# Kernel optimization log

Hardware: AMD Instinct MI355X
Metric: run time of the kernel (lower is better)

The kernel has to match this reference:

```python
import jax, jax.numpy as jnp
import numpy as np

N, D, E = 200000, 256, 6400000
RATIO = 0.5
NEG_SLOPE = 0.2


def _xavier(key, shape, gain=1.414):
    fan_in, fan_out = shape[0], shape[1]
    limit = gain * (6.0 / (fan_in + fan_out)) ** 0.5
    return jax.random.uniform(key, shape, jnp.float32, -limit, limit)


def setup_inputs() -> dict:
    key = jax.random.key(0)
    ks = jax.random.split(key, 8)
    x = jax.random.normal(ks[0], (N, D), jnp.float32)
    edge_index = jax.random.randint(ks[1], (2, E), 0, N, dtype=jnp.int64)
    return {
        "x": x,
        "edge_index": edge_index,
        "w_s1": _xavier(ks[2], (2 * D, D)), "b_s1": jnp.zeros((D,), jnp.float32),
        "w_s2": _xavier(ks[3], (D, 1)),     "b_s2": jnp.zeros((1,), jnp.float32),
        "w_f1": _xavier(ks[4], (D, D // 2)), "b_f1": jnp.zeros((D // 2,), jnp.float32),
        "w_f2": _xavier(ks[5], (D // 2, 1)), "b_f2": jnp.zeros((1,), jnp.float32),
        "w_p": _xavier(ks[6], (D, D)),      "b_p": jnp.zeros((D,), jnp.float32),
        "alpha": jnp.float32(0.5), "beta": jnp.float32(0.5),
    }


def reference(x, edge_index, w_s1, b_s1, w_s2, b_s2, w_f1, b_f1, w_f2, b_f2, w_p, b_p, alpha, beta):
    num_nodes = x.shape[0]
    k = max(1, int(RATIO * num_nodes))
    lrelu = lambda v: jax.nn.leaky_relu(v, NEG_SLOPE)

    row, col = edge_index[0], edge_index[1]
    # degree(row, N): scatter-add of ones over source nodes
    deg = jax.ops.segment_sum(jnp.ones_like(row, dtype=x.dtype), row, num_segments=num_nodes)
    # F.normalize(p=2, dim=0) on the [N,1] degree column
    deg_norm = deg / jnp.maximum(jnp.sqrt(jnp.sum(deg * deg)), 1e-12)

    struct_in = jnp.concatenate([x, jnp.broadcast_to(deg_norm[:, None], x.shape)], axis=1)  # [N, 2D]
    struct_scores = (lrelu(struct_in @ w_s1 + b_s1) @ w_s2 + b_s2)[:, 0]  # dropout is eval no-op
    feat_scores = (lrelu(x @ w_f1 + b_f1) @ w_f2 + b_f2)[:, 0]

    a = jax.nn.sigmoid(alpha)
    b = jax.nn.sigmoid(beta)
    s = a + b
    scores = (a / s) * struct_scores + (b / s) * feat_scores  # [N]

    # single-graph top-k (batch=None default path)
    topk_scores, topk_idx = jax.lax.top_k(scores, k)
    x_pooled = lrelu(x[topk_idx] @ w_p + b_p)  # post_pool, dropout no-op

    # edge remap + compaction (valid edges first, -1 padding to keep static shape)
    node_map = jnp.full((num_nodes,), -1, dtype=jnp.int32).at[topk_idx].set(
        jnp.arange(k, dtype=jnp.int32))
    mr, mc = node_map[row], node_map[col]
    mask = (mr >= 0) & (mc >= 0)
    order = jnp.argsort(~mask, stable=True)  # stable: keeps original edge order among valid
    edge_index_pooled = jnp.stack([
        jnp.where(mask, mr, -1)[order],
        jnp.where(mask, mc, -1)[order],
    ])
    return x_pooled, edge_index_pooled, topk_scores
```

## Files before the change

### kernel.cpp

```cpp
#include <hip/hip_runtime.h>
#include <math.h>

typedef unsigned long long u64;
typedef unsigned int u32;
typedef unsigned short u16;
typedef __attribute__((ext_vector_type(8))) short bf16x8;
typedef __attribute__((ext_vector_type(4))) float f32x4;

#define D   256
#define ECH 16
#define EBLK (256*ECH)
#define BAND_W 2048
#define BAND_DELTA 1e-3f
#define HR  50176
#define HCH 64
#define NBUCK 65536

__device__ __forceinline__ double lrelu(double v){ return v > 0.0 ? v : 0.2*v; }
__device__ __forceinline__ float  lreluf(float v){ return v > 0.0f ? v : 0.2f*v; }

__device__ __forceinline__ u16 f2bf(float f){
  union{float f; u32 u;} v; v.f = f;
  u32 r = v.u + 0x7FFFu + ((v.u >> 16) & 1u);
  return (u16)(r >> 16);
}
__device__ __forceinline__ float bf2f(u16 b){
  union{u32 u; float f;} v; v.u = ((u32)b) << 16; return v.f;
}

__global__ __launch_bounds__(256) void k_deghist(const int* __restrict__ row, int E,
                                                 u32* __restrict__ partial, int NR){
  __shared__ u32 h[HR/4];
  const int tid = threadIdx.x;
  const int r = blockIdx.x % NR;
  const int c = blockIdx.x / NR;
  for (int i = tid; i < HR/4; i += 256) h[i] = 0;
  __syncthreads();
  const int lo = r * HR;
  int CE = ((E + HCH - 1) / HCH + 3) & ~3;
  const int e0 = c * CE;
  const int e1 = min(e0 + CE, E);
  for (int e = e0 + tid*4; e < e1; e += 256*4){
    if (e + 3 < e1){
      int4 v = *(const int4*)(row + e);
      u32 d0 = (u32)(v.x - lo), d1 = (u32)(v.y - lo);
      u32 d2 = (u32)(v.z - lo), d3 = (u32)(v.w - lo);
      if (d0 < (u32)HR) atomicAdd(&h[d0 >> 2], 1u << ((d0 & 3)*8));
      if (d1 < (u32)HR) atomicAdd(&h[d1 >> 2], 1u << ((d1 & 3)*8));
      if (d2 < (u32)HR) atomicAdd(&h[d2 >> 2], 1u << ((d2 & 3)*8));
      if (d3 < (u32)HR) atomicAdd(&h[d3 >> 2], 1u << ((d3 & 3)*8));
    } else {
      for (int j = 0; j < 4 && e + j < e1; ++j){
        u32 d = (u32)(row[e+j] - lo);
        if (d < (u32)HR) atomicAdd(&h[d >> 2], 1u << ((d & 3)*8));
      }
    }
  }
  __syncthreads();
  u32* plane = partial + (size_t)blockIdx.x * (HR/4);
  for (int i = tid; i < HR/4; i += 256) plane[i] = h[i];
}

__global__ void k_degred2(const u32* __restrict__ partial, int N, int NR,
                          int* __restrict__ deg, u64* __restrict__ out){
  __shared__ u64 sh[256];
  u64 local = 0;
  int stride = gridDim.x*blockDim.x;
  for (int i = blockIdx.x*blockDim.x + threadIdx.x; i < N; i += stride){
    int r = i / HR, off = i % HR;
    const int word = off >> 2, shift = (off & 3)*8;
    u32 s = 0;
    #pragma unroll 8
    for (int c = 0; c < HCH; ++c)
      s += (partial[(size_t)(c*NR + r)*(HR/4) + word] >> shift) & 0xFFu;
    deg[i] = (int)s;
    local += (u64)s * (u64)s;
  }
  sh[threadIdx.x] = local; __syncthreads();
  for (int s = 128; s > 0; s >>= 1){
    if (threadIdx.x < s) sh[threadIdx.x] += sh[threadIdx.x+s];
    __syncthreads();
  }
  if (threadIdx.x == 0) atomicAdd(out, sh[0]);
}

__global__ void k_prep_wsw(const float* __restrict__ wS1, const float* __restrict__ wF1,
                           const float* __restrict__ wP,
                           const float* __restrict__ alpha, const float* __restrict__ beta,
                           const u64* __restrict__ sumsq,
                           u16* __restrict__ wswH, u16* __restrict__ wswL,
                           u16* __restrict__ wPH,
                           double* __restrict__ s1b, double* __restrict__ scal,
                           float* __restrict__ s1bf, float* __restrict__ scalf){
  const int b = blockIdx.x;
  if (b < 384){
    int idx = b*256 + threadIdx.x;
    int i    = idx & 7;
    int lane = (idx >> 3) & 63;
    int sg   = (idx >> 9) & 7;
    int t    = idx >> 12;
    int k = sg*32 + ((lane >> 4) & 3)*8 + i;
    int c16 = lane & 15;
    float wv;
    if (t < 16) wv = wS1[k*256 + t*16 + c16];
    else        wv = wF1[k*128 + (t-16)*16 + c16];
    u16 h = f2bf(wv);
    wswH[idx] = h;
    wswL[idx] = f2bf(wv - bf2f(h));
  } else if (b < 640){
    int idx = (b-384)*256 + threadIdx.x;
    int i    = idx & 7;
    int lane = (idx >> 3) & 63;
    int sg   = (idx >> 9) & 7;
    int t    = idx >> 12;
    int k = sg*32 + ((lane >> 4) & 3)*8 + i;
    wPH[idx] = f2bf(wP[k*256 + t*16 + (lane & 15)]);
  } else {
    int j = threadIdx.x;
    double s = 0.0;
    for (int r = 0; r < D; ++r) s += (double)wS1[(D + r)*D + j];
    s1b[j] = s;
    s1bf[j] = (float)s;
    if (j == 0){
      double a = 1.0/(1.0 + exp(-(double)alpha[0]));
      double bb = 1.0/(1.0 + exp(-(double)beta[0]));
      scal[0] = a/(a+bb);
      scal[1] = bb/(a+bb);
      double dn = sqrt((double)(*sumsq));
      scal[2] = dn > 1e-12 ? dn : 1e-12;
      scalf[0] = (float)scal[0];
      scalf[1] = (float)scal[1];
      scalf[2] = (float)(1.0/scal[2]);
    }
  }
}

__global__ __launch_bounds__(512, 4) void k_scores_mfma(
    const float* __restrict__ x, const int* __restrict__ deg,
    const u16* __restrict__ wswH, const u16* __restrict__ wswL,
    const float* __restrict__ bS1, const float* __restrict__ wS2, const float* __restrict__ bS2,
    const float* __restrict__ bF1, const float* __restrict__ wF2, const float* __restrict__ bF2,
    const float* __restrict__ s1bf, const float* __restrict__ scalf,
    float* __restrict__ s32, u64* __restrict__ keysrc, u32* __restrict__ kmm, int N)
{
  __shared__ u16 xsh[2][4096];
  __shared__ u16 xsl[2][4096];
  __shared__ float dnsh[64];
  __shared__ float part_s[64][9];
  __shared__ float part_f[64][9];

  const int tid  = threadIdx.x;
  const int lane = tid & 63;
  const int w    = tid >> 6;
  const int node0 = blockIdx.x * 64;

  if (tid < 64){
    int node = node0 + tid;
    dnsh[tid] = (node < N) ? ((float)deg[node] * scalf[2]) : 0.0f;
  }

  const int row_st = tid >> 3;
  const int seg_st = tid & 7;
  const int unit_w = row_st*8 + (seg_st ^ (row_st & 7));
  const float* srcbase = x + (size_t)(node0 + row_st)*D + seg_st*8;
  const bool rv = (node0 + row_st) < N;

  f32x4 acc[4][3];
  #pragma unroll
  for (int m = 0; m < 4; ++m)
    #pragma unroll
    for (int n = 0; n < 3; ++n) acc[m][n] = (f32x4){0.f,0.f,0.f,0.f};

  float xr[8];
  {
    if (rv){
      float4 a = *(const float4*)(srcbase);
      float4 b = *(const float4*)(srcbase + 4);
      xr[0]=a.x; xr[1]=a.y; xr[2]=a.z; xr[3]=a.w;
      xr[4]=b.x; xr[5]=b.y; xr[6]=b.z; xr[7]=b.w;
    } else {
      #pragma unroll
      for (int i = 0; i < 8; ++i) xr[i] = 0.f;
    }
  }

  #pragma unroll
  for (int c = 0; c < 4; ++c){
    const int pb = c & 1;
    {
      u16 h[8];
      #pragma unroll
      for (int i = 0; i < 8; ++i) h[i] = f2bf(xr[i]);
      uint4 H; H.x = (u32)h[0] | ((u32)h[1]<<16); H.y = (u32)h[2] | ((u32)h[3]<<16);
               H.z = (u32)h[4] | ((u32)h[5]<<16); H.w = (u32)h[6] | ((u32)h[7]<<16);
      u16 l[8];
      #pragma unroll
      for (int i = 0; i < 8; ++i) l[i] = f2bf(xr[i] - bf2f(h[i]));
      uint4 L; L.x = (u32)l[0] | ((u32)l[1]<<16); L.y = (u32)l[2] | ((u32)l[3]<<16);
               L.z = (u32)l[4] | ((u32)l[5]<<16); L.w = (u32)l[6] | ((u32)l[7]<<16);
      *(uint4*)&xsh[pb][unit_w*8] = H;
      *(uint4*)&xsl[pb][unit_w*8] = L;
    }
    __syncthreads();
    if (c < 3){
      const float* sn = srcbase + (c+1)*64;
      if (rv){
        float4 a = *(const float4*)(sn);
        float4 b = *(const float4*)(sn + 4);
        xr[0]=a.x; xr[1]=a.y; xr[2]=a.z; xr[3]=a.w;
        xr[4]=b.x; xr[5]=b.y; xr[6]=b.z; xr[7]=b.w;
      }
    }
    #pragma unroll
    for (int s = 0; s < 2; ++s){
      const int sg = c*2 + s;
      bf16x8 ah[4], al[4];
      #pragma unroll
      for (int mt = 0; mt < 4; ++mt){
        int row = mt*16 + (lane & 15);
        int seg = s*4 + (lane >> 4);
        int un  = row*8 + (seg ^ (row & 7));
        ah[mt] = *(const bf16x8*)&xsh[pb][un*8];
        al[mt] = *(const bf16x8*)&xsl[pb][un*8];
      }
      const int t0 = w*3;
      size_t o0 = ((size_t)(t0*8 + sg)*64 + lane)*8;
      bf16x8 bh = *(const bf16x8*)&wswH[o0];
      bf16x8 bl = *(const bf16x8*)&wswL[o0];
      #pragma unroll
      for (int nt = 0; nt < 3; ++nt){
        bf16x8 nbh = bh, nbl = bl;
        if (nt < 2){
          size_t on = ((size_t)((t0+nt+1)*8 + sg)*64 + lane)*8;
          nbh = *(const bf16x8*)&wswH[on];
          nbl = *(const bf16x8*)&wswL[on];
        }
        #pragma unroll
        for (int mt = 0; mt < 4; ++mt){
          acc[mt][nt] = __builtin_amdgcn_mfma_f32_16x16x32_bf16(ah[mt], bh, acc[mt][nt], 0,0,0);
          acc[mt][nt] = __builtin_amdgcn_mfma_f32_16x16x32_bf16(al[mt], bh, acc[mt][nt], 0,0,0);
          acc[mt][nt] = __builtin_amdgcn_mfma_f32_16x16x32_bf16(ah[mt], bl, acc[mt][nt], 0,0,0);
        }
        bh = nbh; bl = nbl;
      }
    }
    if (c < 3) __syncthreads();
  }

  float dnl[4][4];
  #pragma unroll
  for (int mt = 0; mt < 4; ++mt)
    #pragma unroll
    for (int j = 0; j < 4; ++j)
      dnl[mt][j] = dnsh[mt*16 + (lane>>4)*4 + j];

  float ps[4][4], pf[4][4];
  #pragma unroll
  for (int mt = 0; mt < 4; ++mt)
    #pragma unroll
    for (int j = 0; j < 4; ++j){ ps[mt][j] = 0.f; pf[mt][j] = 0.f; }

  #pragma unroll
  for (int nt = 0; nt < 3; ++nt){
    const int t = w*3 + nt;
    const int c16 = lane & 15;
    const bool isS = (t < 16);
    const int col = isS ? t*16 + c16 : (t-16)*16 + c16;
    const float bias = isS ? bS1[col] : bF1[col];
    const float sbv  = isS ? s1bf[col] : 0.f;
    const float vv   = isS ? wS2[col] : wF2[col];
    #pragma unroll
    for (int mt = 0; mt < 4; ++mt){
      #pragma unroll
      for (int j = 0; j < 4; ++j){
        float v = acc[mt][nt][j] + bias + dnl[mt][j]*sbv;
        v = lreluf(v) * vv;
        v += __shfl_xor(v, 1);
        v += __shfl_xor(v, 2);
        v += __shfl_xor(v, 4);
        v += __shfl_xor(v, 8);
        if (isS) ps[mt][j] += v; else pf[mt][j] += v;
      }
    }
  }
  if ((lane & 15) == 0){
    #pragma unroll
    for (int mt = 0; mt < 4; ++mt)
      #pragma unroll
      for (int j = 0; j < 4; ++j){
        int row = mt*16 + (lane>>4)*4 + j;
        part_s[row][w] = ps[mt][j];
        part_f[row][w] = pf[mt][j];
      }
  }
  __syncthreads();
  if (tid < 64){
    int node = node0 + tid;
    u32 key32mn = 0xFFFFFFFFu, key32mx = 0u;
    if (node < N){
      float sv = 0.f, fv = 0.f;
      #pragma unroll
      for (int ww = 0; ww < 8; ++ww){ sv += part_s[tid][ww]; fv += part_f[tid][ww]; }
      float sc = scalf[0]*(sv + bS2[0]) + scalf[1]*(fv + bF2[0]);
      s32[node] = sc;
      u32 bits = __float_as_uint(sc);
      u32 ord = (bits >> 31) ? ~bits : (bits | 0x80000000u);
      u32 key32 = ~ord;
      keysrc[node] = ((u64)key32 << 32) | (u32)node;
      key32mn = key32; key32mx = key32;
    }
    #pragma unroll
    for (int off = 32; off > 0; off >>= 1){
      u32 on = __shfl_xor(key32mn, off);
      u32 ox = __shfl_xor(key32mx, off);
      key32mn = min(key32mn, on);
      key32mx = max(key32mx, ox);
    }
    if (tid == 0){
      atomicMin(&kmm[0], key32mn);
      atomicMax(&kmm[1], key32mx);
    }
  }
}

__global__ void k_hist(const u64* __restrict__ keysrc, int N,
                       const u32* __restrict__ kmm, u32* __restrict__ hist){
  const u32 kmin = kmm[0];
  const u64 rng = (u64)(kmm[1] - kmm[0]) + 1;
  int stride = gridDim.x*blockDim.x;
  for (int i = blockIdx.x*blockDim.x + threadIdx.x; i < N; i += stride){
    u32 key = (u32)(keysrc[i] >> 32);
    u32 b = (u32)((((u64)(key - kmin)) << 16) / rng);
    atomicAdd(&hist[b], 1u);
  }
}

__global__ __launch_bounds__(1024) void k_scan64k(const u32* __restrict__ hist,
                                                  u32* __restrict__ boff){
  __shared__ u32 ts[1024];
  const int t = threadIdx.x;
  u32 loc[64];
  u32 s = 0;
  const uint4* hp = (const uint4*)(hist + t*64);
  #pragma unroll
  for (int i = 0; i < 16; ++i){
    uint4 v = hp[i];
    loc[i*4+0]=v.x; loc[i*4+1]=v.y; loc[i*4+2]=v.z; loc[i*4+3]=v.w;
    s += v.x + v.y + v.z + v.w;
  }
  ts[t] = s; __syncthreads();
  for (int d = 1; d < 1024; d <<= 1){
    u32 v = (t >= d) ? ts[t-d] : 0;
    __syncthreads();
    ts[t] += v;
    __syncthreads();
  }
  u32 run = ts[t] - s;
  u32* bp = boff + t*64;
  #pragma unroll 8
  for (int i = 0; i < 64; ++i){ bp[i] = run; run += loc[i]; }
}

__global__ void k_scatter(const u64* __restrict__ keysrc, int N,
                          const u32* __restrict__ kmm, u32* __restrict__ boff,
                          u64* __restrict__ keyS){
  const u32 kmin = kmm[0];
  const u64 rng = (u64)(kmm[1] - kmm[0]) + 1;
  int stride = gridDim.x*blockDim.x;
  for (int i = blockIdx.x*blockDim.x + threadIdx.x; i < N; i += stride){
    u64 kv = keysrc[i];
    u32 key = (u32)(kv >> 32);
    u32 b = (u32)((((u64)(key - kmin)) << 16) / rng);
    u32 pos = atomicAdd(&boff[b], 1u);
    keyS[pos] = kv;
  }
}

__global__ void kr_cut(const u64* __restrict__ keys, int k, float* __restrict__ cutbuf,
                       int* __restrict__ r01){
  if (threadIdx.x == 0 && blockIdx.x == 0){
    u32 key32 = (u32)(keys[k-1] >> 32);
    u32 ord = ~key32;
    u32 u = (ord & 0x80000000u) ? (ord ^ 0x80000000u) : ~ord;
    float c = __uint_as_float(u);
    cutbuf[0] = c - BAND_DELTA;
    cutbuf[1] = c + BAND_DELTA;
    r01[0] = 0x7FFFFFFF;
    r01[1] = -1;
  }
}

__global__ __launch_bounds__(256) void kr_rescore(
    const u64* __restrict__ keys, const float* __restrict__ s32,
    const float* __restrict__ x, const int* __restrict__ deg,
    const float* __restrict__ wS1, const float* __restrict__ bS1,
    const float* __restrict__ wS2, const float* __restrict__ bS2,
    const float* __restrict__ wF1, const float* __restrict__ bF1,
    const float* __restrict__ wF2, const float* __restrict__ bF2,
    const double* __restrict__ s1b, const double* __restrict__ scal,
    const float* __restrict__ cutbuf, int* __restrict__ r01,
    double* __restrict__ bandS, int k, int N)
{
  const int r = k - BAND_W + blockIdx.x;
  if (r < 0 || r >= N) return;
  const int node = (int)(u32)(keys[r] & 0xFFFFFFFFULL);
  const float s = s32[node];
  if (s < cutbuf[0] || s > cutbuf[1]){
    if (threadIdx.x == 0) bandS[blockIdx.x] = (double)s;
    return;
  }

  const int tid = threadIdx.x;
  if (tid == 0){ atomicMin(&r01[0], r); atomicMax(&r01[1], r); }

  __shared__ float xr[256];
  __shared__ double rsp[4], rfp[4];
  xr[tid] = x[(size_t)node*D + tid];
  __syncthreads();

  const int j = tid;
  double a0=0.0, a1=0.0, a2=0.0, a3=0.0;
  double b0=0.0, b1=0.0, b2=0.0, b3=0.0;
  if (j < 128){
    for (int rr = 0; rr < D; rr += 4){
      double x0 = (double)xr[rr+0], x1 = (double)xr[rr+1];
      double x2 = (double)xr[rr+2], x3 = (double)xr[rr+3];
      a0 = fma(x0, (double)wS1[(rr+0)*D + j], a0);
      a1 = fma(x1, (double)wS1[(rr+1)*D + j], a1);
      a2 = fma(x2, (double)wS1[(rr+2)*D + j], a2);
      a3 = fma(x3, (double)wS1[(rr+3)*D + j], a3);
      b0 = fma(x0, (double)wF1[(rr+0)*128 + j], b0);
      b1 = fma(x1, (double)wF1[(rr+1)*128 + j], b1);
      b2 = fma(x2, (double)wF1[(rr+2)*128 + j], b2);
      b3 = fma(x3, (double)wF1[(rr+3)*128 + j], b3);
    }
  } else {
    for (int rr = 0; rr < D; rr += 4){
      double x0 = (double)xr[rr+0], x1 = (double)xr[rr+1];
      double x2 = (double)xr[rr+2], x3 = (double)xr[rr+3];
      a0 = fma(x0, (double)wS1[(rr+0)*D + j], a0);
      a1 = fma(x1, (double)wS1[(rr+1)*D + j], a1);
      a2 = fma(x2, (double)wS1[(rr+2)*D + j], a2);
      a3 = fma(x3, (double)wS1[(rr+3)*D + j], a3);
    }
  }
  double accA = ((a0+a1)+(a2+a3)) + (double)bS1[j] + ((double)deg[node]/scal[2]) * s1b[j];
  double sp = lrelu(accA) * (double)wS2[j];
  double fp = 0.0;
  if (j < 128){
    double accB = ((b0+b1)+(b2+b3)) + (double)bF1[j];
    fp = lrelu(accB) * (double)wF2[j];
  }

  const int lane = tid & 63, wave = tid >> 6;
  #pragma unroll
  for (int off = 32; off > 0; off >>= 1){
    sp += __shfl_down(sp, off);
    fp += __shfl_down(fp, off);
  }
  if (lane == 0){ rsp[wave] = sp; rfp[wave] = fp; }
  __syncthreads();
  if (tid == 0){
    double SP = rsp[0]+rsp[1]+rsp[2]+rsp[3];
    double FP = rfp[0]+rfp[1]+rfp[2]+rfp[3];
    bandS[blockIdx.x] = scal[0]*(SP + (double)bS2[0]) + scal[1]*(FP + (double)bF2[0]);
  }
}

__global__ __launch_bounds__(1024) void kr_bandsort(u64* __restrict__ keys,
    const double* __restrict__ bandS, const int* __restrict__ r01, int k){
  __shared__ double bs[4096];
  __shared__ int bi[4096];
  const int r0 = r01[0], r1 = r01[1];
  int nb = r1 - r0 + 1;
  if (nb <= 1) return;
  if (nb > 4096) nb = 4096;
  int M = 1; while (M < nb) M <<= 1;
  const int tid = threadIdx.x;
  const int sbase = r0 - (k - BAND_W);
  for (int m = tid; m < M; m += 1024){
    if (m < nb){ bs[m] = bandS[sbase + m]; bi[m] = (int)(u32)(keys[r0+m] & 0xFFFFFFFFULL); }
    else       { bs[m] = -1.0/0.0;         bi[m] = 0x7FFFFFFF; }
  }
  __syncthreads();
  for (int size = 2; size <= M; size <<= 1){
    for (int stride = size >> 1; stride > 0; stride >>= 1){
      for (int p = tid; p < (M >> 1); p += 1024){
        int i = 2*p - (p & (stride-1));
        int jj = i + stride;
        bool up = ((i & size) == 0);
        double si_ = bs[i], sj = bs[jj];
        int ii = bi[i], ij = bi[jj];
        bool gt = (si_ < sj) || (si_ == sj && ii > ij);
        if (gt == up){ bs[i]=sj; bs[jj]=si_; bi[i]=ij; bi[jj]=ii; }
      }
      __syncthreads();
    }
  }
  for (int m = tid; m < nb; m += 1024)
    keys[r0+m] = (u64)(u32)bi[m];
}

__global__ void k_finalize(const u64* __restrict__ keys, const float* __restrict__ s32,
                           int k, int* __restrict__ nmap, float* __restrict__ outS){
  int p = blockIdx.x*blockDim.x + threadIdx.x;
  if (p < k){
    int node = (int)(u32)(keys[p] & 0xFFFFFFFFULL);
    nmap[node] = p;
    outS[p] = s32[node];
  }
}

__global__ __launch_bounds__(512, 4) void k_xpool_mfma(
    const float* __restrict__ x, const u64* __restrict__ keys,
    const u16* __restrict__ wH,
    const float* __restrict__ bP, float* __restrict__ out, int kk)
{
  __shared__ u16 xsh[2][4096];

  const int tid  = threadIdx.x;
  const int lane = tid & 63;
  const int w    = tid >> 6;
  const int p0 = blockIdx.x * 64;
  if (p0 >= kk) return;

  const int row_st = tid >> 3;
  const int seg_st = tid & 7;
  const int unit_w = row_st*8 + (seg_st ^ (row_st & 7));
  int prow = p0 + row_st; if (prow >= kk) prow = kk - 1;
  const int node = (int)(u32)(keys[prow] & 0xFFFFFFFFULL);
  const float* srcbase = x + (size_t)node*D + seg_st*8;

  f32x4 acc[4][2];
  #pragma unroll
  for (int m = 0; m < 4; ++m){ acc[m][0] = (f32x4){0.f,0.f,0.f,0.f}; acc[m][1] = (f32x4){0.f,0.f,0.f,0.f}; }

  float xr[8];
  {
    float4 a = *(const float4*)(srcbase);
    float4 b = *(const float4*)(srcbase + 4);
    xr[0]=a.x; xr[1]=a.y; xr[2]=a.z; xr[3]=a.w;
    xr[4]=b.x; xr[5]=b.y; xr[6]=b.z; xr[7]=b.w;
  }

  #pragma unroll
  for (int c = 0; c < 4; ++c){
    const int pb = c & 1;
    {
      u16 h[8];
      #pragma unroll
      for (int i = 0; i < 8; ++i) h[i] = f2bf(xr[i]);
      uint4 H; H.x = (u32)h[0] | ((u32)h[1]<<16); H.y = (u32)h[2] | ((u32)h[3]<<16);
               H.z = (u32)h[4] | ((u32)h[5]<<16); H.w = (u32)h[6] | ((u32)h[7]<<16);
      *(uint4*)&xsh[pb][unit_w*8] = H;
    }
    __syncthreads();
    if (c < 3){
      const float* sn = srcbase + (c+1)*64;
      float4 a = *(const float4*)(sn);
      float4 b = *(const float4*)(sn + 4);
      xr[0]=a.x; xr[1]=a.y; xr[2]=a.z; xr[3]=a.w;
      xr[4]=b.x; xr[5]=b.y; xr[6]=b.z; xr[7]=b.w;
    }
    #pragma unroll
    for (int s = 0; s < 2; ++s){
      const int sg = c*2 + s;
      bf16x8 ah[4];
      #pragma unroll
      for (int mt = 0; mt < 4; ++mt){
        int row = mt*16 + (lane & 15);
        int seg = s*4 + (lane >> 4);
        int un  = row*8 + (seg ^ (row & 7));
        ah[mt] = *(const bf16x8*)&xsh[pb][un*8];
      }
      const int t0 = w*2;
      size_t o0 = ((size_t)(t0*8 + sg)*64 + lane)*8;
      bf16x8 bh = *(const bf16x8*)&wH[o0];
      #pragma unroll
      for (int nt = 0; nt < 2; ++nt){
        bf16x8 nbh = bh;
        if (nt < 1){
          size_t on = ((size_t)((t0+1)*8 + sg)*64 + lane)*8;
          nbh = *(const bf16x8*)&wH[on];
        }
        #pragma unroll
        for (int mt = 0; mt < 4; ++mt)
          acc[mt][nt] = __builtin_amdgcn_mfma_f32_16x16x32_bf16(ah[mt], bh, acc[mt][nt], 0,0,0);
        bh = nbh;
      }
    }
    if (c < 3) __syncthreads();
  }

  const int c16 = lane & 15, r4 = (lane >> 4)*4;
  #pragma unroll
  for (int nt = 0; nt < 2; ++nt){
    const int col = (w*2 + nt)*16 + c16;
    const float bias = bP[col];
    #pragma unroll
    for (int mt = 0; mt < 4; ++mt){
      #pragma unroll
      for (int j = 0; j < 4; ++j){
        int p = p0 + mt*16 + r4 + j;
        if (p < kk) out[(size_t)p*D + col] = lreluf(acc[mt][nt][j] + bias);
      }
    }
  }
}

__global__ __launch_bounds__(256) void k_ecount(const int* __restrict__ erow, const int* __restrict__ ecol,
    const int* __restrict__ nmap, int E, int* __restrict__ bcount){
  __shared__ int sc[256];
  const int tid = threadIdx.x;
  const int base = blockIdx.x*EBLK + tid*ECH;
  int cnt = 0;
  #pragma unroll
  for (int q = 0; q < ECH; ++q){
    int e = base + q;
    if (e < E){
      if (nmap[erow[e]] >= 0 && nmap[ecol[e]] >= 0) cnt++;
    }
  }
  sc[tid] = cnt; __syncthreads();
  for (int s = 128; s > 0; s >>= 1){
    if (tid < s) sc[tid] += sc[tid+s];
    __syncthreads();
  }
  if (tid == 0) bcount[blockIdx.x] = sc[0];
}

__global__ __launch_bounds__(1024) void k_escan(const int* __restrict__ bcount, int nblk,
                                                int* __restrict__ boff, int* __restrict__ tot){
  __shared__ int sh[1024];
  const int tid = threadIdx.x;
  int carry = 0;
  for (int s = 0; s < nblk; s += 1024){
    int v = (s + tid < nblk) ? bcount[s+tid] : 0;
    sh[tid] = v; __syncthreads();
    for (int d = 1; d < 1024; d <<= 1){
      int t = (tid >= d) ? sh[tid-d] : 0;
      __syncthreads();
      sh[tid] += t;
      __syncthreads();
    }
    if (s + tid < nblk) boff[s+tid] = carry + sh[tid] - v;
    carry += sh[1023];
    __syncthreads();
  }
  if (tid == 0) *tot = carry;
}

__global__ void k_efill_tail(float* __restrict__ outR, float* __restrict__ outC,
                             const int* __restrict__ tot, int E){
  const int t0 = *tot;
  int stride = gridDim.x*blockDim.x;
  for (int i = t0 + blockIdx.x*blockDim.x + threadIdx.x; i < E; i += stride){
    outR[i] = -1.0f;
    outC[i] = -1.0f;
  }
}

__global__ __launch_bounds__(256) void k_escatter(const int* __restrict__ erow, const int* __restrict__ ecol,
    const int* __restrict__ nmap, int E, const int* __restrict__ boff,
    float* __restrict__ outR, float* __restrict__ outC){
  __shared__ int sc[256];
  const int tid = threadIdx.x;
  const int base = blockIdx.x*EBLK + tid*ECH;
  int mr[ECH], mc[ECH];
  int cnt = 0;
  #pragma unroll
  for (int q = 0; q < ECH; ++q){
    int e = base + q;
    int a = -1, b = -1;
    if (e < E){ a = nmap[erow[e]]; b = nmap[ecol[e]]; }
    mr[q] = a; mc[q] = b;
    if (a >= 0 && b >= 0) cnt++;
  }
  sc[tid] = cnt; __syncthreads();
  int v = cnt;
  for (int d = 1; d < 256; d <<= 1){
    int t = (tid >= d) ? sc[tid-d] : 0;
    __syncthreads();
    sc[tid] += t;
    __syncthreads();
  }
  int pos = boff[blockIdx.x] + sc[tid] - v;
  #pragma unroll
  for (int q = 0; q < ECH; ++q){
    if (mr[q] >= 0 && mc[q] >= 0){
      outR[pos] = (float)mr[q];
      outC[pos] = (float)mc[q];
      pos++;
    }
  }
}

extern "C" void kernel_launch(void* const* d_in, const int* in_sizes, int n_in,
                              void* d_out, int out_size, void* d_ws, size_t ws_size,
                              hipStream_t stream)
{
  const float* x   = (const float*)d_in[0];
  const int*   ei  = (const int*)d_in[1];
  const float* wS1 = (const float*)d_in[2];
  const float* bS1 = (const float*)d_in[3];
  const float* wS2 = (const float*)d_in[4];
  const float* bS2 = (const float*)d_in[5];
  const float* wF1 = (const float*)d_in[6];
  const float* bF1 = (const float*)d_in[7];
  const float* wF2 = (const float*)d_in[8];
  const float* bF2 = (const float*)d_in[9];
  const float* wP  = (const float*)d_in[10];
  const float* bP  = (const float*)d_in[11];
  const float* alpha = (const float*)d_in[12];
  const float* beta  = (const float*)d_in[13];
  (void)n_in; (void)out_size; (void)ws_size;

  const int N = in_sizes[0] / D;
  const int E = in_sizes[1] / 2;
  int k = (int)(0.5 * (double)N); if (k < 1) k = 1;
  const int nblk_e = (E + EBLK - 1) / EBLK;
  const int NR = (N + HR - 1) / HR;

  char* w = (char*)d_ws;
  size_t off = 0;
  auto alloc = [&](size_t bytes)->char*{
    char* p = w + off;
    off = (off + bytes + 255) & ~(size_t)255;
    return p;
  };
  float*  s32    = (float*) alloc((size_t)N*4);
  u64*    keysrc = (u64*)   alloc((size_t)N*8);
  u64*    keyS   = (u64*)   alloc((size_t)N*8);
  int*    deg    = (int*)   alloc((size_t)N*4);
  int*    nmap   = (int*)   alloc((size_t)N*4);
  u32*    kmm    = (u32*)   alloc(2*4);
  u32*    hist   = (u32*)   alloc((size_t)NBUCK*4);
  u32*    boffH  = (u32*)   alloc((size_t)NBUCK*4);
  double* s1b    = (double*)alloc((size_t)D*8);
  float*  s1bf   = (float*) alloc((size_t)D*4);
  double* scal   = (double*)alloc(4*8);
  float*  scalf  = (float*) alloc(4*4);
  u64*    sumsq  = (u64*)   alloc(8);
  float*  cutbuf = (float*) alloc(2*4);
  int*    r01    = (int*)   alloc(2*4);
  int*    tot    = (int*)   alloc(4);
  double* bandS  = (double*)alloc((size_t)2*BAND_W*8);
  u16*    wswH   = (u16*)   alloc((size_t)98304*2);
  u16*    wswL   = (u16*)   alloc((size_t)98304*2);
  u16*    wswPH  = (u16*)   alloc((size_t)65536*2);
  int*    bcount = (int*)   alloc((size_t)nblk_e*4);
  int*    boff   = (int*)   alloc((size_t)nblk_e*4);

  float* outX  = (float*)d_out;
  float* outER = outX  + (size_t)k*D;
  float* outEC = outER + (size_t)E;
  float* outS  = outEC + (size_t)E;

  u32* partial = (u32*)outER;

  hipMemsetAsync(sumsq, 0,    8,               stream);
  hipMemsetAsync(nmap,  0xFF, (size_t)N*4,     stream);
  hipMemsetAsync(kmm,   0xFF, 4,               stream);
  hipMemsetAsync(kmm+1, 0x00, 4,               stream);
  hipMemsetAsync(hist,  0,    (size_t)NBUCK*4, stream);

  k_deghist<<<NR*HCH, 256, 0, stream>>>(ei, E, partial, NR);
  k_degred2<<<1024, 256, 0, stream>>>(partial, N, NR, deg, sumsq);
  k_prep_wsw<<<641, 256, 0, stream>>>(wS1, wF1, wP, alpha, beta, sumsq,
                                      wswH, wswL, wswPH,
                                      s1b, scal, s1bf, scalf);
  k_scores_mfma<<<(N + 63)/64, 512, 0, stream>>>(x, deg, wswH, wswL,
                                                 bS1, wS2, bS2, bF1, wF2, bF2,
                                                 s1bf, scalf, s32, keysrc, kmm, N);

  k_hist   <<<(N+255)/256, 256, 0, stream>>>(keysrc, N, kmm, hist);
  k_scan64k<<<1, 1024, 0, stream>>>(hist, boffH);
  k_scatter<<<(N+255)/256, 256, 0, stream>>>(keysrc, N, kmm, boffH, keyS);

  kr_cut     <<<1, 64, 0, stream>>>(keyS, k, cutbuf, r01);
  kr_rescore <<<2*BAND_W, 256, 0, stream>>>(keyS, s32, x, deg, wS1,bS1,wS2,bS2,
                                            wF1,bF1,wF2,bF2, s1b, scal,
                                            cutbuf, r01, bandS, k, N);
  kr_bandsort<<<1, 1024, 0, stream>>>(keyS, bandS, r01, k);

  k_finalize<<<(k+255)/256, 256, 0, stream>>>(keyS, s32, k, nmap, outS);
  k_xpool_mfma<<<(k+63)/64, 512, 0, stream>>>(x, keyS, wswPH, bP, outX, k);
  k_ecount  <<<nblk_e, 256, 0, stream>>>(ei, ei+E, nmap, E, bcount);
  k_escan   <<<1, 1024, 0, stream>>>(bcount, nblk_e, boff, tot);
  k_efill_tail<<<1024, 256, 0, stream>>>(outER, outEC, tot, E);
  k_escatter<<<nblk_e, 256, 0, stream>>>(ei, ei+E, nmap, E, boff, outER, outEC);
}
```

Baseline: 690.0 us.

## Fuse edge count, scan and scatter into single-pass decoupled look-back kernel

```diff
diff --git a/kernel.cpp b/kernel.cpp
--- a/kernel.cpp
+++ b/kernel.cpp
@@ -608,46 +608,64 @@
   }
 }
 
-__global__ __launch_bounds__(256) void k_ecount(const int* __restrict__ erow, const int* __restrict__ ecol,
-    const int* __restrict__ nmap, int E, int* __restrict__ bcount){
+__global__ __launch_bounds__(256) void k_edges(const int* __restrict__ erow,
+    const int* __restrict__ ecol, const int* __restrict__ nmap, int E,
+    u32* __restrict__ ticket, u64* __restrict__ flags, int nblk,
+    float* __restrict__ outR, float* __restrict__ outC, int* __restrict__ tot){
   __shared__ int sc[256];
+  __shared__ int stk;
+  __shared__ int sprefix;
   const int tid = threadIdx.x;
-  const int base = blockIdx.x*EBLK + tid*ECH;
+  if (tid == 0) stk = (int)atomicAdd(ticket, 1u);
+  __syncthreads();
+  const int tk = stk;
+  const int base = tk*EBLK + tid*ECH;
+  int mr[ECH], mc[ECH];
   int cnt = 0;
   #pragma unroll
   for (int q = 0; q < ECH; ++q){
     int e = base + q;
-    if (e < E){
-      if (nmap[erow[e]] >= 0 && nmap[ecol[e]] >= 0) cnt++;
-    }
+    int a = -1, b = -1;
+    if (e < E){ a = nmap[erow[e]]; b = nmap[ecol[e]]; }
+    mr[q] = a; mc[q] = b;
+    if (a >= 0 && b >= 0) cnt++;
   }
   sc[tid] = cnt; __syncthreads();
-  for (int s = 128; s > 0; s >>= 1){
-    if (tid < s) sc[tid] += sc[tid+s];
+  int v = cnt;
+  for (int d = 1; d < 256; d <<= 1){
+    int t = (tid >= d) ? sc[tid-d] : 0;
     __syncthreads();
-  }
-  if (tid == 0) bcount[blockIdx.x] = sc[0];
-}
-
-__global__ __launch_bounds__(1024) void k_escan(const int* __restrict__ bcount, int nblk,
-                                                int* __restrict__ boff, int* __restrict__ tot){
-  __shared__ int sh[1024];
-  const int tid = threadIdx.x;
-  int carry = 0;
-  for (int s = 0; s < nblk; s += 1024){
-    int v = (s + tid < nblk) ? bcount[s+tid] : 0;
-    sh[tid] = v; __syncthreads();
-    for (int d = 1; d < 1024; d <<= 1){
-      int t = (tid >= d) ? sh[tid-d] : 0;
-      __syncthreads();
-      sh[tid] += t;
-      __syncthreads();
-    }
-    if (s + tid < nblk) boff[s+tid] = carry + sh[tid] - v;
-    carry += sh[1023];
+    sc[tid] += t;
     __syncthreads();
   }
-  if (tid == 0) *tot = carry;
+  const u32 total = (u32)sc[255];
+  if (tid == 0){
+    __hip_atomic_store(&flags[tk], (1ULL << 62) | (u64)total,
+                       __ATOMIC_RELEASE, __HIP_MEMORY_SCOPE_AGENT);
+    u32 run = 0;
+    for (int j = tk - 1; j >= 0; --j){
+      u64 f;
+      do {
+        f = __hip_atomic_load(&flags[j], __ATOMIC_ACQUIRE, __HIP_MEMORY_SCOPE_AGENT);
+      } while ((f >> 62) == 0);
+      run += (u32)(f & 0x3FFFFFFFFFFFFFFFULL);
+      if ((f >> 62) == 2ULL) break;
+    }
+    __hip_atomic_store(&flags[tk], (2ULL << 62) | (u64)(run + total),
+                       __ATOMIC_RELEASE, __HIP_MEMORY_SCOPE_AGENT);
+    sprefix = (int)run;
+    if (tk == nblk - 1) *tot = (int)(run + total);
+  }
+  __syncthreads();
+  int pos = sprefix + sc[tid] - v;
+  #pragma unroll
+  for (int q = 0; q < ECH; ++q){
+    if (mr[q] >= 0 && mc[q] >= 0){
+      outR[pos] = (float)mr[q];
+      outC[pos] = (float)mc[q];
+      pos++;
+    }
+  }
 }
 
 __global__ void k_efill_tail(float* __restrict__ outR, float* __restrict__ outC,
@@ -657,41 +675,6 @@
   for (int i = t0 + blockIdx.x*blockDim.x + threadIdx.x; i < E; i += stride){
     outR[i] = -1.0f;
     outC[i] = -1.0f;
-  }
-}
-
-__global__ __launch_bounds__(256) void k_escatter(const int* __restrict__ erow, const int* __restrict__ ecol,
-    const int* __restrict__ nmap, int E, const int* __restrict__ boff,
-    float* __restrict__ outR, float* __restrict__ outC){
-  __shared__ int sc[256];
-  const int tid = threadIdx.x;
-  const int base = blockIdx.x*EBLK + tid*ECH;
-  int mr[ECH], mc[ECH];
-  int cnt = 0;
-  #pragma unroll
-  for (int q = 0; q < ECH; ++q){
-    int e = base + q;
-    int a = -1, b = -1;
-    if (e < E){ a = nmap[erow[e]]; b = nmap[ecol[e]]; }
-    mr[q] = a; mc[q] = b;
-    if (a >= 0 && b >= 0) cnt++;
-  }
-  sc[tid] = cnt; __syncthreads();
-  int v = cnt;
-  for (int d = 1; d < 256; d <<= 1){
-    int t = (tid >= d) ? sc[tid-d] : 0;
-    __syncthreads();
-    sc[tid] += t;
-    __syncthreads();
-  }
-  int pos = boff[blockIdx.x] + sc[tid] - v;
-  #pragma unroll
-  for (int q = 0; q < ECH; ++q){
-    if (mr[q] >= 0 && mc[q] >= 0){
-      outR[pos] = (float)mr[q];
-      outC[pos] = (float)mc[q];
-      pos++;
-    }
   }
 }
 
@@ -744,12 +727,12 @@
   float*  cutbuf = (float*) alloc(2*4);
   int*    r01    = (int*)   alloc(2*4);
   int*    tot    = (int*)   alloc(4);
+  u32*    ticket = (u32*)   alloc(4);
+  u64*    flags  = (u64*)   alloc((size_t)nblk_e*8);
   double* bandS  = (double*)alloc((size_t)2*BAND_W*8);
   u16*    wswH   = (u16*)   alloc((size_t)98304*2);
   u16*    wswL   = (u16*)   alloc((size_t)98304*2);
   u16*    wswPH  = (u16*)   alloc((size_t)65536*2);
-  int*    bcount = (int*)   alloc((size_t)nblk_e*4);
-  int*    boff   = (int*)   alloc((size_t)nblk_e*4);
 
   float* outX  = (float*)d_out;
   float* outER = outX  + (size_t)k*D;
@@ -758,11 +741,13 @@
 
   u32* partial = (u32*)outER;
 
-  hipMemsetAsync(sumsq, 0,    8,               stream);
-  hipMemsetAsync(nmap,  0xFF, (size_t)N*4,     stream);
-  hipMemsetAsync(kmm,   0xFF, 4,               stream);
-  hipMemsetAsync(kmm+1, 0x00, 4,               stream);
-  hipMemsetAsync(hist,  0,    (size_t)NBUCK*4, stream);
+  hipMemsetAsync(sumsq,  0,    8,               stream);
+  hipMemsetAsync(nmap,   0xFF, (size_t)N*4,     stream);
+  hipMemsetAsync(kmm,    0xFF, 4,               stream);
+  hipMemsetAsync(kmm+1,  0x00, 4,               stream);
+  hipMemsetAsync(hist,   0,    (size_t)NBUCK*4, stream);
+  hipMemsetAsync(ticket, 0,    4,               stream);
+  hipMemsetAsync(flags,  0,    (size_t)nblk_e*8, stream);
 
   k_deghist<<<NR*HCH, 256, 0, stream>>>(ei, E, partial, NR);
   k_degred2<<<1024, 256, 0, stream>>>(partial, N, NR, deg, sumsq);
@@ -785,8 +770,8 @@
 
   k_finalize<<<(k+255)/256, 256, 0, stream>>>(keyS, s32, k, nmap, outS);
   k_xpool_mfma<<<(k+63)/64, 512, 0, stream>>>(x, keyS, wswPH, bP, outX, k);
-  k_ecount  <<<nblk_e, 256, 0, stream>>>(ei, ei+E, nmap, E, bcount);
-  k_escan   <<<1, 1024, 0, stream>>>(bcount, nblk_e, boff, tot);
+
+  k_edges<<<nblk_e, 256, 0, stream>>>(ei, ei+E, nmap, E, ticket, flags, nblk_e,
+                                      outER, outEC, tot);
   k_efill_tail<<<1024, 256, 0, stream>>>(outER, outEC, tot, E);
-  k_escatter<<<nblk_e, 256, 0, stream>>>(ei, ei+E, nmap, E, boff, outER, outEC);
-}
+}
```

Result: slower. 1.303 ms (+88.8%).
